# Performance work log

Measured on AMD Instinct MI355X. Metric: run time of the kernel, lower is better.

## Reference

```python
import jax, jax.numpy as jnp
import numpy as np

GAMMA = 1.0

def setup_inputs() -> dict:
    key = jax.random.key(0)
    kx, ky = jax.random.split(key)
    x = jax.random.normal(kx, (8192, 256), dtype=jnp.float32)
    y = jax.random.normal(ky, (8192, 256), dtype=jnp.float32)
    return {"x": x, "y": y}

def reference(x, y):
    # RBF kernel K[i,j] = exp(-gamma * ||x_i - y_j||^2)
    # materializing the O(N*M*D) broadcast difference tensor.
    x2 = jnp.sum(x * x, axis=-1)            # [N]
    y2 = jnp.sum(y * y, axis=-1)            # [M]
    xy = jnp.einsum('nd,md->nm', x, y)      # [N, M] GEMM
    dist2 = x2[:, None] + y2[None, :] - 2.0 * xy
    dist2 = jnp.maximum(dist2, 0.0)         # guard tiny negative round-off
    return jnp.exp(-GAMMA * dist2)
```

## Files before the change

kernel.cpp:

```cpp
#include <hip/hip_runtime.h>


#define M_DIM 8192
#define K_DIM 256
#define BM 64
#define BN 64
#define NT 16

typedef __attribute__((ext_vector_type(4))) float float4v;
typedef __attribute__((ext_vector_type(4))) int   int4v;
typedef __attribute__((ext_vector_type(8))) int   int8v;

__global__ __launch_bounds__(256) void prep_kernel(
        const float* __restrict__ x, const float* __restrict__ y,
        unsigned char* __restrict__ xb, unsigned char* __restrict__ yb,
        float* __restrict__ x2, float* __restrict__ y2) {
    int row  = blockIdx.x * 4 + (threadIdx.x >> 6);
    int lane = threadIdx.x & 63;

    const float* src; unsigned char* dst; float* nrm; int r;
    if (row < M_DIM) { src = x; dst = xb; nrm = x2; r = row; }
    else             { src = y; dst = yb; nrm = y2; r = row - M_DIM; }

    const float4* s4 = (const float4*)(src + (size_t)r * K_DIM);
    float4 v = s4[lane];
    float ss = v.x * v.x + v.y * v.y + v.z * v.z + v.w * v.w;

    int packed = __builtin_amdgcn_cvt_pk_fp8_f32(v.x, v.y, 0, false);
    packed     = __builtin_amdgcn_cvt_pk_fp8_f32(v.z, v.w, packed, true);

    int u  = lane >> 2;
    int su = u ^ (r & 15);
    *(unsigned int*)(dst + (size_t)r * 256 + su * 16 + (lane & 3) * 4) =
        (unsigned int)packed;

    #pragma unroll
    for (int o = 32; o > 0; o >>= 1) ss += __shfl_down(ss, o);
    if (lane == 0) nrm[r] = ss;
}

__global__ __launch_bounds__(256, 4) void rbf_gemm(
        const unsigned char* __restrict__ xb, const unsigned char* __restrict__ yb,
        const float* __restrict__ x2, const float* __restrict__ y2,
        float* __restrict__ out) {
    __shared__ __align__(16) unsigned char Bs[2][BN * 256];
    __shared__ __align__(16) float y2s[NT * BN];

    const int tid  = threadIdx.x;
    const int wid  = tid >> 6;
    const int lane = tid & 63;
    const int wm   = wid >> 1;
    const int wn   = wid & 1;

    const int bid = blockIdx.x;
    const int xcd = bid & 7;
    const int lin = bid >> 3;
    const int ty  = (xcd << 4) + (lin >> 3);
    const int tx0 = (lin & 7) << 4;
    const int m0  = ty * BM;

    const int fr = lane & 15;
    const int g  = lane >> 4;
    const int q  = lane >> 4;
    const int c  = lane & 15;

    #pragma unroll
    for (int i = 0; i < 4; ++i) {
        const int ch = wid * 4 + i;
        __builtin_amdgcn_global_load_lds(
            (__attribute__((address_space(1))) void*)
                (yb + (size_t)(tx0 * BN + ch * 4) * 256 + lane * 16),
            (__attribute__((address_space(3))) void*)&Bs[0][ch * 1024],
            16, 0, 0);
    }
    __builtin_amdgcn_global_load_lds(
        (__attribute__((address_space(1))) void*)
            ((const unsigned char*)(y2 + tx0 * BN) + wid * 1024 + lane * 16),
        (__attribute__((address_space(3))) void*)
            ((unsigned char*)y2s + wid * 1024 + lane * 16),
        16, 0, 0);

    int8v a[2][2];
    #pragma unroll
    for (int mt = 0; mt < 2; ++mt) {
        const unsigned char* ar =
            xb + (size_t)(m0 + wm * 32 + mt * 16 + fr) * 256;
        #pragma unroll
        for (int ks = 0; ks < 2; ++ks) {
            const int p0 = 8 * ks + 2 * g;
            int4v lo = *(const int4v*)(ar + ((p0 ^ fr) << 4));
            int4v hi = *(const int4v*)(ar + (((p0 + 1) ^ fr) << 4));
            a[mt][ks] = (int8v){lo.x, lo.y, lo.z, lo.w,
                                hi.x, hi.y, hi.z, hi.w};
        }
    }
    float x2s[2];
    #pragma unroll
    for (int mt = 0; mt < 2; ++mt)
        x2s[mt] = x2[m0 + wm * 32 + mt * 16 + c];

    __syncthreads();

    int cur = 0;
    for (int t = 0; t < NT; ++t) {
        const int n0 = (tx0 + t) * BN;

        if (t + 1 < NT) {
            const int n1 = (tx0 + t + 1) * BN;
            #pragma unroll
            for (int i = 0; i < 4; ++i) {
                const int ch = wid * 4 + i;
                __builtin_amdgcn_global_load_lds(
                    (__attribute__((address_space(1))) void*)
                        (yb + (size_t)(n1 + ch * 4) * 256 + lane * 16),
                    (__attribute__((address_space(3))) void*)
                        &Bs[cur ^ 1][ch * 1024],
                    16, 0, 0);
            }
        }

        float4v y2q[2];
        #pragma unroll
        for (int nt = 0; nt < 2; ++nt)
            y2q[nt] = *(const float4v*)
                &y2s[t * BN + wn * 32 + nt * 16 + q * 4];

        int8v b[2][2];
        #pragma unroll
        for (int ks = 0; ks < 2; ++ks) {
            const int p0 = 8 * ks + 2 * g;
            const int u0 = ((p0 ^ fr) << 4);
            const int u1 = (((p0 + 1) ^ fr) << 4);
            #pragma unroll
            for (int nt = 0; nt < 2; ++nt) {
                const int rb = (wn * 32 + nt * 16 + fr) * 256;
                int4v lo = *(const int4v*)&Bs[cur][rb + u0];
                int4v hi = *(const int4v*)&Bs[cur][rb + u1];
                b[nt][ks] = (int8v){lo.x, lo.y, lo.z, lo.w,
                                    hi.x, hi.y, hi.z, hi.w};
            }
        }

        float4v acc[2][2] = {};
        #pragma unroll
        for (int ks = 0; ks < 2; ++ks)
            #pragma unroll
            for (int mt = 0; mt < 2; ++mt)
                #pragma unroll
                for (int nt = 0; nt < 2; ++nt)
                    acc[mt][nt] =
                        __builtin_amdgcn_mfma_scale_f32_16x16x128_f8f6f4(
                            b[nt][ks], a[mt][ks], acc[mt][nt],
                            0, 0, 0, 0x7F, 0, 0x7F);

        #pragma unroll
        for (int mt = 0; mt < 2; ++mt) {
            const size_t rowbase =
                (size_t)(m0 + wm * 32 + mt * 16 + c) * M_DIM;
            #pragma unroll
            for (int nt = 0; nt < 2; ++nt) {
                float dv[4];
                #pragma unroll
                for (int v = 0; v < 4; ++v) {
                    float d = x2s[mt] + y2q[nt][v] - 2.0f * acc[mt][nt][v];
                    dv[v] = fmaxf(d, 0.0f);
                }
                float4v r = {0.0f, 0.0f, 0.0f, 0.0f};
                bool anylt = (dv[0] < 105.0f) | (dv[1] < 105.0f) |
                             (dv[2] < 105.0f) | (dv[3] < 105.0f);
                if (__ballot(anylt) != 0ULL) {
                    #pragma unroll
                    for (int v = 0; v < 4; ++v)
                        r[v] = (dv[v] < 105.0f) ? __expf(-dv[v]) : 0.0f;
                }
                *(float4v*)&out[rowbase + n0 + wn * 32 + nt * 16 + q * 4] = r;
            }
        }

        if (t + 1 < NT) {
            asm volatile("s_waitcnt vmcnt(4)\n\ts_barrier" ::: "memory");
            cur ^= 1;
        }
    }
}

__global__ void rbf_naive(const float* __restrict__ x, const float* __restrict__ y,
                          float* __restrict__ out) {
    __shared__ float xs[16][17];
    __shared__ float ys[16][17];
    const int tx = threadIdx.x, ty = threadIdx.y;
    const int row = blockIdx.y * 16 + ty;
    const int col = blockIdx.x * 16 + tx;
    float acc = 0.0f;
    for (int k0 = 0; k0 < K_DIM; k0 += 16) {
        xs[ty][tx] = x[(size_t)row * K_DIM + k0 + tx];
        ys[ty][tx] = y[(size_t)(blockIdx.x * 16 + ty) * K_DIM + k0 + tx];
        __syncthreads();
        #pragma unroll
        for (int kk = 0; kk < 16; ++kk) {
            float d = xs[ty][kk] - ys[tx][kk];
            acc += d * d;
        }
        __syncthreads();
    }
    out[(size_t)row * M_DIM + col] = __expf(-acc);
}

extern "C" void kernel_launch(void* const* d_in, const int* in_sizes, int n_in,
                              void* d_out, int out_size, void* d_ws, size_t ws_size,
                              hipStream_t stream) {
    const float* x = (const float*)d_in[0];
    const float* y = (const float*)d_in[1];
    float* out = (float*)d_out;

    const size_t need = (size_t)2 * M_DIM * 256
                      + (size_t)2 * M_DIM * sizeof(float);
    if (ws_size >= need) {
        unsigned char* xb = (unsigned char*)d_ws;
        unsigned char* yb = xb + (size_t)M_DIM * 256;
        float* x2 = (float*)(yb + (size_t)M_DIM * 256);
        float* y2 = x2 + M_DIM;

        prep_kernel<<<dim3((2 * M_DIM) / 4), dim3(256), 0, stream>>>(x, y, xb, yb, x2, y2);
        rbf_gemm<<<dim3((M_DIM / BM) * (M_DIM / BN) / NT), dim3(256), 0, stream>>>(xb, yb, x2, y2, out);
    } else {
        rbf_naive<<<dim3(M_DIM / 16, M_DIM / 16), dim3(16, 16), 0, stream>>>(x, y, out);
    }
}
```

Measured before the change: 291.5 us.

## Retile RBF GEMM to 16x512 blocks and defer the exp epilogue

The output tile per block changes from 64 rows by 16 sequential 64-column tiles to 16 rows by 512 columns. Each wave now owns one 16-column slice and keeps eight accumulators across the y sweep. The exp/store epilogue runs once after all MFMA work instead of being interleaved with each tile. This multiplies the grid size by eight and raises the amount of y data each block stages per output element. A full __syncthreads each step likely also waits for the prefetch just issued, which removes the load/compute overlap the old partial vmcnt wait allowed.

New measurement: 318.8 us. 9.3% more time.

```diff
diff --git a/kernel.cpp b/kernel.cpp
--- a/kernel.cpp
+++ b/kernel.cpp
@@ -3,9 +3,9 @@
 
 #define M_DIM 8192
 #define K_DIM 256
-#define BM 64
-#define BN 64
-#define NT 16
+#define BM 16
+#define BN 512
+#define NSUB 8
 
 typedef __attribute__((ext_vector_type(4))) float float4v;
 typedef __attribute__((ext_vector_type(4))) int   int4v;
@@ -43,21 +43,20 @@
         const unsigned char* __restrict__ xb, const unsigned char* __restrict__ yb,
         const float* __restrict__ x2, const float* __restrict__ y2,
         float* __restrict__ out) {
-    __shared__ __align__(16) unsigned char Bs[2][BN * 256];
-    __shared__ __align__(16) float y2s[NT * BN];
+    __shared__ __align__(16) unsigned char Bs[2][64 * 256];
+    __shared__ __align__(16) float y2s[BN];
 
     const int tid  = threadIdx.x;
     const int wid  = tid >> 6;
     const int lane = tid & 63;
-    const int wm   = wid >> 1;
-    const int wn   = wid & 1;
-
-    const int bid = blockIdx.x;
-    const int xcd = bid & 7;
-    const int lin = bid >> 3;
-    const int ty  = (xcd << 4) + (lin >> 3);
-    const int tx0 = (lin & 7) << 4;
-    const int m0  = ty * BM;
+
+    const int bid   = blockIdx.x;
+    const int xcd   = bid & 7;
+    const int lin   = bid >> 3;
+    const int panel = (xcd << 1) | (lin >> 9);
+    const int rowt  = lin & 511;
+    const int m0    = rowt * BM;
+    const int n0    = panel * BN;
 
     const int fr = lane & 15;
     const int g  = lane >> 4;
@@ -69,118 +68,90 @@
         const int ch = wid * 4 + i;
         __builtin_amdgcn_global_load_lds(
             (__attribute__((address_space(1))) void*)
-                (yb + (size_t)(tx0 * BN + ch * 4) * 256 + lane * 16),
+                (yb + (size_t)(n0 + ch * 4) * 256 + lane * 16),
             (__attribute__((address_space(3))) void*)&Bs[0][ch * 1024],
             16, 0, 0);
     }
-    __builtin_amdgcn_global_load_lds(
-        (__attribute__((address_space(1))) void*)
-            ((const unsigned char*)(y2 + tx0 * BN) + wid * 1024 + lane * 16),
-        (__attribute__((address_space(3))) void*)
-            ((unsigned char*)y2s + wid * 1024 + lane * 16),
-        16, 0, 0);
-
-    int8v a[2][2];
-    #pragma unroll
-    for (int mt = 0; mt < 2; ++mt) {
-        const unsigned char* ar =
-            xb + (size_t)(m0 + wm * 32 + mt * 16 + fr) * 256;
+    if (wid < 2) {
+        __builtin_amdgcn_global_load_lds(
+            (__attribute__((address_space(1))) void*)
+                ((const unsigned char*)(y2 + n0) + wid * 1024 + lane * 16),
+            (__attribute__((address_space(3))) void*)
+                ((unsigned char*)y2s + wid * 1024 + lane * 16),
+            16, 0, 0);
+    }
+
+    int8v a[2];
+    {
+        const unsigned char* ar = xb + (size_t)(m0 + fr) * 256;
         #pragma unroll
         for (int ks = 0; ks < 2; ++ks) {
             const int p0 = 8 * ks + 2 * g;
             int4v lo = *(const int4v*)(ar + ((p0 ^ fr) << 4));
             int4v hi = *(const int4v*)(ar + (((p0 + 1) ^ fr) << 4));
-            a[mt][ks] = (int8v){lo.x, lo.y, lo.z, lo.w,
-                                hi.x, hi.y, hi.z, hi.w};
-        }
-    }
-    float x2s[2];
-    #pragma unroll
-    for (int mt = 0; mt < 2; ++mt)
-        x2s[mt] = x2[m0 + wm * 32 + mt * 16 + c];
+            a[ks] = (int8v){lo.x, lo.y, lo.z, lo.w, hi.x, hi.y, hi.z, hi.w};
+        }
+    }
+    const float x2v = x2[m0 + c];
 
     __syncthreads();
 
+    float4v acc[NSUB] = {};
     int cur = 0;
-    for (int t = 0; t < NT; ++t) {
-        const int n0 = (tx0 + t) * BN;
-
-        if (t + 1 < NT) {
-            const int n1 = (tx0 + t + 1) * BN;
+
+    for (int it = 0; it < NSUB; ++it) {
+        if (it + 1 < NSUB) {
+            const int nr = n0 + (it + 1) * 64;
             #pragma unroll
             for (int i = 0; i < 4; ++i) {
                 const int ch = wid * 4 + i;
                 __builtin_amdgcn_global_load_lds(
                     (__attribute__((address_space(1))) void*)
-                        (yb + (size_t)(n1 + ch * 4) * 256 + lane * 16),
+                        (yb + (size_t)(nr + ch * 4) * 256 + lane * 16),
                     (__attribute__((address_space(3))) void*)
                         &Bs[cur ^ 1][ch * 1024],
                     16, 0, 0);
             }
         }
 
-        float4v y2q[2];
-        #pragma unroll
-        for (int nt = 0; nt < 2; ++nt)
-            y2q[nt] = *(const float4v*)
-                &y2s[t * BN + wn * 32 + nt * 16 + q * 4];
-
-        int8v b[2][2];
+        int8v b[2];
         #pragma unroll
         for (int ks = 0; ks < 2; ++ks) {
             const int p0 = 8 * ks + 2 * g;
-            const int u0 = ((p0 ^ fr) << 4);
-            const int u1 = (((p0 + 1) ^ fr) << 4);
+            const int rb = (wid * 16 + fr) * 256;
+            int4v lo = *(const int4v*)&Bs[cur][rb + ((p0 ^ fr) << 4)];
+            int4v hi = *(const int4v*)&Bs[cur][rb + (((p0 + 1) ^ fr) << 4)];
+            b[ks] = (int8v){lo.x, lo.y, lo.z, lo.w, hi.x, hi.y, hi.z, hi.w};
+        }
+
+        acc[it] = __builtin_amdgcn_mfma_scale_f32_16x16x128_f8f6f4(
+            b[0], a[0], acc[it], 0, 0, 0, 0x7F, 0, 0x7F);
+        acc[it] = __builtin_amdgcn_mfma_scale_f32_16x16x128_f8f6f4(
+            b[1], a[1], acc[it], 0, 0, 0, 0x7F, 0, 0x7F);
+
+        __syncthreads();
+        cur ^= 1;
+    }
+
+    const size_t rowbase = (size_t)(m0 + c) * M_DIM + n0;
+    #pragma unroll
+    for (int it = 0; it < NSUB; ++it) {
+        const float4v y2q = *(const float4v*)&y2s[it * 64 + wid * 16 + q * 4];
+        float dv[4];
+        #pragma unroll
+        for (int v = 0; v < 4; ++v) {
+            float d = x2v + y2q[v] - 2.0f * acc[it][v];
+            dv[v] = fmaxf(d, 0.0f);
+        }
+        float4v r = {0.0f, 0.0f, 0.0f, 0.0f};
+        bool anylt = (dv[0] < 105.0f) | (dv[1] < 105.0f) |
+                     (dv[2] < 105.0f) | (dv[3] < 105.0f);
+        if (__ballot(anylt) != 0ULL) {
             #pragma unroll
-            for (int nt = 0; nt < 2; ++nt) {
-                const int rb = (wn * 32 + nt * 16 + fr) * 256;
-                int4v lo = *(const int4v*)&Bs[cur][rb + u0];
-                int4v hi = *(const int4v*)&Bs[cur][rb + u1];
-                b[nt][ks] = (int8v){lo.x, lo.y, lo.z, lo.w,
-                                    hi.x, hi.y, hi.z, hi.w};
-            }
-        }
-
-        float4v acc[2][2] = {};
-        #pragma unroll
-        for (int ks = 0; ks < 2; ++ks)
-            #pragma unroll
-            for (int mt = 0; mt < 2; ++mt)
-                #pragma unroll
-                for (int nt = 0; nt < 2; ++nt)
-                    acc[mt][nt] =
-                        __builtin_amdgcn_mfma_scale_f32_16x16x128_f8f6f4(
-                            b[nt][ks], a[mt][ks], acc[mt][nt],
-                            0, 0, 0, 0x7F, 0, 0x7F);
-
-        #pragma unroll
-        for (int mt = 0; mt < 2; ++mt) {
-            const size_t rowbase =
-                (size_t)(m0 + wm * 32 + mt * 16 + c) * M_DIM;
-            #pragma unroll
-            for (int nt = 0; nt < 2; ++nt) {
-                float dv[4];
-                #pragma unroll
-                for (int v = 0; v < 4; ++v) {
-                    float d = x2s[mt] + y2q[nt][v] - 2.0f * acc[mt][nt][v];
-                    dv[v] = fmaxf(d, 0.0f);
-                }
-                float4v r = {0.0f, 0.0f, 0.0f, 0.0f};
-                bool anylt = (dv[0] < 105.0f) | (dv[1] < 105.0f) |
-                             (dv[2] < 105.0f) | (dv[3] < 105.0f);
-                if (__ballot(anylt) != 0ULL) {
-                    #pragma unroll
-                    for (int v = 0; v < 4; ++v)
-                        r[v] = (dv[v] < 105.0f) ? __expf(-dv[v]) : 0.0f;
-                }
-                *(float4v*)&out[rowbase + n0 + wn * 32 + nt * 16 + q * 4] = r;
-            }
-        }
-
-        if (t + 1 < NT) {
-            asm volatile("s_waitcnt vmcnt(4)\n\ts_barrier" ::: "memory");
-            cur ^= 1;
-        }
+            for (int v = 0; v < 4; ++v)
+                r[v] = (dv[v] < 105.0f) ? __expf(-dv[v]) : 0.0f;
+        }
+        *(float4v*)&out[rowbase + it * 64 + wid * 16 + q * 4] = r;
     }
 }
 
@@ -222,7 +193,7 @@
         float* y2 = x2 + M_DIM;
 
         prep_kernel<<<dim3((2 * M_DIM) / 4), dim3(256), 0, stream>>>(x, y, xb, yb, x2, y2);
-        rbf_gemm<<<dim3((M_DIM / BM) * (M_DIM / BN) / NT), dim3(256), 0, stream>>>(xb, yb, x2, y2, out);
+        rbf_gemm<<<dim3((M_DIM / BM) * (M_DIM / BN)), dim3(256), 0, stream>>>(xb, yb, x2, y2, out);
     } else {
         rbf_naive<<<dim3(M_DIM / 16, M_DIM / 16), dim3(16, 16), 0, stream>>>(x, y, out);
     }
```
